# Performance work log

Hardware: AMD Instinct MI355X
Metric: run time of the kernel (lower is better)

The kernel has to match this reference:

```python
import jax, jax.numpy as jnp
import numpy as np

N_HEADS = 16


def setup_inputs() -> dict:
    key = jax.random.key(0)
    ks = jax.random.split(key, 9)
    B, S, D = 2, 2048, 1024
    s = 0.02
    return {
        "x": jax.random.normal(ks[0], (B, S, D), dtype=jnp.float32),
        "Wq": jax.random.normal(ks[1], (D, D), dtype=jnp.float32) * s,
        "bq": jax.random.normal(ks[2], (D,), dtype=jnp.float32) * s,
        "Wk": jax.random.normal(ks[3], (D, D), dtype=jnp.float32) * s,
        "bk": jax.random.normal(ks[4], (D,), dtype=jnp.float32) * s,
        "Wv": jax.random.normal(ks[5], (D, D), dtype=jnp.float32) * s,
        "bv": jax.random.normal(ks[6], (D,), dtype=jnp.float32) * s,
        "Wo": jax.random.normal(ks[7], (D, D), dtype=jnp.float32) * s,
        "bo": jax.random.normal(ks[8], (D,), dtype=jnp.float32) * s,
    }


def reference(x, Wq, bq, Wk, bk, Wv, bv, Wo, bo):
    B, S, D = x.shape
    H = N_HEADS
    hd = D // H
    # projections -> [B, H, S, hd]
    def heads(w, b):
        return (x @ w + b).reshape(B, S, H, hd).transpose(0, 2, 1, 3)
    Q, K, V = heads(Wq, bq), heads(Wk, bk), heads(Wv, bv)
    scores = jnp.einsum("bhqd,bhkd->bhqk", Q, K)
    causal = jnp.triu(jnp.ones((S, S), dtype=bool), k=1)  # True above diagonal
    scores = jnp.where(causal, -jnp.inf, scores)
    w = jax.nn.softmax(scores / jnp.sqrt(jnp.float32(hd)), axis=-1)
    ctx = jnp.einsum("bhqk,bhkd->bhqd", w, V).transpose(0, 2, 1, 3).reshape(B, S, D)
    return ctx @ Wo + bo
```

## Files before the change

### kernel.cpp

```cpp
#include <hip/hip_runtime.h>
#include <hip/hip_bf16.h>

typedef __attribute__((ext_vector_type(8))) short short8;
typedef __attribute__((ext_vector_type(4))) float floatx4;
typedef __attribute__((ext_vector_type(4))) int intx4;

#define D_MODEL 1024
#define SEQ     2048
#define NB      2
#define NH      16
#define HD      64
#define MROWS   4096
#define CZ      (0.125f * 1.44269504f)

__device__ __forceinline__ floatx4 mfma_bf16(short8 a, short8 b, floatx4 c) {
  return __builtin_amdgcn_mfma_f32_16x16x32_bf16(a, b, c, 0, 0, 0);
}

__device__ __forceinline__ void dma16(const __hip_bfloat16* g, __hip_bfloat16* l) {
  __builtin_amdgcn_global_load_lds(
      (const __attribute__((address_space(1))) void*)g,
      (__attribute__((address_space(3))) void*)l, 16, 0, 0);
}
#define WAIT_VM(n)  __asm__ __volatile__("s_waitcnt vmcnt(" #n ")" ::: "memory")
#define BARRIER()   __asm__ __volatile__("s_barrier" ::: "memory")
#define WAIT_LGKM() __asm__ __volatile__("s_waitcnt lgkmcnt(0)" ::: "memory")

__device__ __forceinline__ int pack2bf(float a, float b) {
  unsigned ua = __builtin_bit_cast(unsigned, a) + 0x8000u;
  unsigned ub = __builtin_bit_cast(unsigned, b) + 0x8000u;
  return (int)__builtin_amdgcn_perm(ub, ua, 0x07060302u);
}

__global__ void prep_kernel(const float* __restrict__ x, __hip_bfloat16* __restrict__ xb,
                            const float* __restrict__ W0, const float* __restrict__ W1,
                            const float* __restrict__ W2, const float* __restrict__ W3,
                            __hip_bfloat16* __restrict__ T0, __hip_bfloat16* __restrict__ T1,
                            __hip_bfloat16* __restrict__ T2, __hip_bfloat16* __restrict__ T3) {
  const int z = blockIdx.z;
  if (z == 4) {
    const int tid = threadIdx.y * 32 + threadIdx.x;
    const int base = ((blockIdx.y * 32 + blockIdx.x) * 256 + tid) * 16;
#pragma unroll
    for (int c = 0; c < 4; c++) {
      float4 v = *(const float4*)(x + base + c * 4);
      __hip_bfloat16 tmp[4];
      tmp[0] = __float2bfloat16(v.x);
      tmp[1] = __float2bfloat16(v.y);
      tmp[2] = __float2bfloat16(v.z);
      tmp[3] = __float2bfloat16(v.w);
      *(ushort4*)(xb + base + c * 4) = *(ushort4*)tmp;
    }
    return;
  }
  const float* W = (z == 0) ? W0 : (z == 1) ? W1 : (z == 2) ? W2 : W3;
  __hip_bfloat16* Wt = (z == 0) ? T0 : (z == 1) ? T1 : (z == 2) ? T2 : T3;
  __shared__ float tile[32][33];
  int k0 = blockIdx.x * 32, n0 = blockIdx.y * 32;
  int tx = threadIdx.x, ty = threadIdx.y;
#pragma unroll
  for (int i = 0; i < 4; i++)
    tile[ty + 8 * i][tx] = W[(size_t)(k0 + ty + 8 * i) * D_MODEL + n0 + tx];
  __syncthreads();
#pragma unroll
  for (int i = 0; i < 4; i++)
    Wt[(size_t)(n0 + ty + 8 * i) * D_MODEL + k0 + tx] = __float2bfloat16(tile[tx][ty + 8 * i]);
}

template <int MODE>
__global__ __launch_bounds__(256) void gemm_kernel(
    const __hip_bfloat16* __restrict__ X,
    const __hip_bfloat16* __restrict__ Wt0, const __hip_bfloat16* __restrict__ Wt1,
    const __hip_bfloat16* __restrict__ Wt2,
    const float* __restrict__ b0, const float* __restrict__ b1, const float* __restrict__ b2,
    void* __restrict__ out0, void* __restrict__ out1, void* __restrict__ out2) {
  constexpr int MT = (MODE == 0) ? 128 : 64;
  constexpr int I = MT / 32;
  constexpr int NKT = D_MODEL / 32;
  constexpr int SMEM_BYTES = 3 * (MT * 32 + 128 * 32) * 2;

  const int z = blockIdx.y;
  const __hip_bfloat16* Wt = (z == 0) ? Wt0 : (z == 1) ? Wt1 : Wt2;
  const float* bias = (z == 0) ? b0 : (z == 1) ? b1 : b2;
  void* outp = (z == 0) ? out0 : (z == 1) ? out1 : out2;
  const float scale = (MODE == 0 && z == 0) ? CZ : 1.f;

  __shared__ __attribute__((aligned(16))) char smem[SMEM_BYTES];
  __hip_bfloat16* As = (__hip_bfloat16*)smem;
  __hip_bfloat16* Bs = (__hip_bfloat16*)smem + 3 * MT * 32;
  float* Es = (float*)smem;

  const int n0 = blockIdx.x * 128;
  const int m0 = blockIdx.z * MT;
  const int t = threadIdx.x;
  const int lane = t & 63, w = t >> 6;
  const int wm = (w >> 1) * (MT / 2), wn = (w & 1) * 64;
  const int lr = lane & 15;
  const int lq = lane >> 4;

  const __hip_bfloat16* Xp = X + (size_t)m0 * D_MODEL;
  const __hip_bfloat16* Wp = Wt + (size_t)n0 * D_MODEL;

  const int lrow = lane >> 2;
  const int skg = (lane & 3) << 3;
  const int srowA = ((MT == 128) ? (w << 5) : (w << 4)) + lrow;
  const int sbA0 = (((MT == 128) ? (w << 5) : (w << 4)) << 5);
  const int sbA1 = sbA0 + (16 << 5);
  const int srowB = (w << 5) + lrow;
  const int sbB0 = ((w << 5) << 5);
  const int sbB1 = sbB0 + (16 << 5);

#define STAGE_G(kt_, buf_)                                                              \
  {                                                                                     \
    const int kn_ = (kt_) * 32;                                                         \
    __hip_bfloat16* A_ = As + (buf_) * (MT * 32);                                       \
    __hip_bfloat16* B_ = Bs + (buf_) * (128 * 32);                                      \
    dma16(Xp + (size_t)srowA * D_MODEL + kn_ + skg, A_ + sbA0);                         \
    if (MT == 128) dma16(Xp + (size_t)(srowA + 16) * D_MODEL + kn_ + skg, A_ + sbA1);   \
    dma16(Wp + (size_t)srowB * D_MODEL + kn_ + skg, B_ + sbB0);                         \
    dma16(Wp + (size_t)(srowB + 16) * D_MODEL + kn_ + skg, B_ + sbB1);                  \
  }

  floatx4 acc[I][4];
#pragma unroll
  for (int i = 0; i < I; i++)
#pragma unroll
    for (int j = 0; j < 4; j++) acc[i][j] = (floatx4){0.f, 0.f, 0.f, 0.f};

  STAGE_G(0, 0);
  STAGE_G(1, 1);

  int cb = 0;
  for (int kt = 0; kt < NKT; kt++) {
    if (kt < NKT - 1) {
      if constexpr (MODE == 0) WAIT_VM(4);
      else                     WAIT_VM(3);
    } else {
      WAIT_VM(0);
    }
    BARRIER();
    if (kt + 2 < NKT) {
      const int nb = (cb == 0) ? 2 : cb - 1;
      STAGE_G(kt + 2, nb);
    }
    const __hip_bfloat16* Ac = As + cb * (MT * 32);
    const __hip_bfloat16* Bc = Bs + cb * (128 * 32);
    short8 af[I], bfr[4];
#pragma unroll
    for (int i = 0; i < I; i++) af[i] = *(const short8*)&Ac[(wm + i * 16 + lr) * 32 + lq * 8];
#pragma unroll
    for (int j = 0; j < 4; j++) bfr[j] = *(const short8*)&Bc[(wn + j * 16 + lr) * 32 + lq * 8];
#pragma unroll
    for (int i = 0; i < I; i++)
#pragma unroll
      for (int j = 0; j < 4; j++) acc[i][j] = mfma_bf16(af[i], bfr[j], acc[i][j]);
    cb = (cb == 2) ? 0 : cb + 1;
  }
#undef STAGE_G

  float bvj[4];
#pragma unroll
  for (int j = 0; j < 4; j++) bvj[j] = bias[n0 + wn + j * 16 + lr];

  if constexpr (MODE == 1) {
    BARRIER();
#pragma unroll
    for (int i = 0; i < I; i++) {
      const int rowb = wm + i * 16 + lq * 4;
#pragma unroll
      for (int j = 0; j < 4; j++)
#pragma unroll
        for (int r = 0; r < 4; r++)
          Es[(rowb + r) * 132 + wn + j * 16 + lr] = acc[i][j][r] + bvj[j];
    }
    WAIT_LGKM();
    BARRIER();
    const int L = t >> 2, nseg = (t & 3) * 32;
    float* op = (float*)outp + (size_t)(m0 + L) * D_MODEL + n0 + nseg;
    const float* src = &Es[L * 132 + nseg];
#pragma unroll
    for (int k = 0; k < 8; k++) *(float4*)(op + 4 * k) = *(const float4*)(src + 4 * k);
  } else if (z != 2) {
    for (int c = 0; c < 2; c++) {
      BARRIER();
#pragma unroll
      for (int i2 = 0; i2 < 2; i2++) {
        const int i = 2 * c + i2;
        const int rowb = (w >> 1) * 32 + i2 * 16 + lq * 4;
#pragma unroll
        for (int j = 0; j < 4; j++)
#pragma unroll
          for (int r = 0; r < 4; r++)
            Es[(rowb + r) * 132 + wn + j * 16 + lr] = (acc[i][j][r] + bvj[j]) * scale;
      }
      WAIT_LGKM();
      BARRIER();
      const int L = t >> 2, nseg = (t & 3) * 32;
      const int m = m0 + ((L >> 5) << 6) + (c << 5) + (L & 31);
      const int bb = m >> 11, s = m & 2047;
      const int nn = n0 + nseg;
      __hip_bfloat16* op = (__hip_bfloat16*)outp +
          (((size_t)(bb * NH + (nn >> 6)) * SEQ + s) * HD + (nn & 63));
      const float* src = &Es[L * 132 + nseg];
#pragma unroll
      for (int k = 0; k < 4; k++) {
        intx4 pk;
        pk[0] = pack2bf(src[8 * k + 0], src[8 * k + 1]);
        pk[1] = pack2bf(src[8 * k + 2], src[8 * k + 3]);
        pk[2] = pack2bf(src[8 * k + 4], src[8 * k + 5]);
        pk[3] = pack2bf(src[8 * k + 6], src[8 * k + 7]);
        *(intx4*)(op + 8 * k) = pk;
      }
    }
  } else {
    for (int c = 0; c < 2; c++) {
      BARRIER();
#pragma unroll
      for (int j2 = 0; j2 < 2; j2++) {
        const int j = 2 * c + j2;
        const int nl = ((w & 1) << 5) + (j2 << 4) + lr;
#pragma unroll
        for (int i = 0; i < I; i++) {
          const int moff = (w >> 1) * 64 + i * 16 + lq * 4;
          floatx4 v = acc[i][j];
          v[0] += bvj[j]; v[1] += bvj[j]; v[2] += bvj[j]; v[3] += bvj[j];
          *(floatx4*)&Es[nl * 132 + moff] = v;
        }
      }
      WAIT_LGKM();
      BARRIER();
      const int nl = t >> 2, mseg = (t & 3) * 32;
      const int n = n0 + ((nl >> 5) << 6) + (c << 5) + (nl & 31);
      const int s0 = m0 & 2047, bb = m0 >> 11;
      __hip_bfloat16* op = (__hip_bfloat16*)outp +
          (((size_t)(bb * NH + (n >> 6)) * HD + (n & 63)) * SEQ + s0 + mseg);
      const float* src = &Es[nl * 132 + mseg];
#pragma unroll
      for (int k = 0; k < 4; k++) {
        intx4 pk;
        pk[0] = pack2bf(src[8 * k + 0], src[8 * k + 1]);
        pk[1] = pack2bf(src[8 * k + 2], src[8 * k + 3]);
        pk[2] = pack2bf(src[8 * k + 4], src[8 * k + 5]);
        pk[3] = pack2bf(src[8 * k + 6], src[8 * k + 7]);
        *(intx4*)(op + 8 * k) = pk;
      }
    }
  }
}

__global__ __launch_bounds__(256, 4) void attn_kernel(
    const __hip_bfloat16* __restrict__ Q, const __hip_bfloat16* __restrict__ Kg,
    const __hip_bfloat16* __restrict__ Vt, __hip_bfloat16* __restrict__ ctx) {
  const int bh = blockIdx.x;
  const int b = bh >> 4, h = bh & 15;
  const int qt = 31 - blockIdx.y;
  const int t = threadIdx.x, lane = t & 63, w = t >> 6;
  const int lr = lane & 15, lq = lane >> 4;
  const int wr = w & 1, wb = w >> 1;

  __shared__ __attribute__((aligned(16))) __hip_bfloat16 Ks[2][64 * 64];
  __shared__ __attribute__((aligned(16))) __hip_bfloat16 VTs[2][64 * 64];

  const __hip_bfloat16* Qb = Q + (size_t)bh * SEQ * HD;
  const __hip_bfloat16* Kb = Kg + (size_t)bh * SEQ * HD;
  const __hip_bfloat16* Vb = Vt + (size_t)bh * HD * SEQ;

  const int qrow0 = qt * 64 + wr * 32;

  short8 qf[2][2];
#pragma unroll
  for (int rt = 0; rt < 2; rt++)
#pragma unroll
    for (int ks = 0; ks < 2; ks++)
      qf[rt][ks] = *(const short8*)(Qb + (size_t)(qrow0 + rt * 16 + lr) * HD + ks * 32 + lq * 8);

  const int srow = (w << 4) + (lane >> 3);
  const int sgl = lane & 7;
  const int sb0 = (w << 4) << 6;
  const int sb1 = ((w << 4) + 8) << 6;

#define STAGE(tb, nb)                                                                  \
  {                                                                                    \
    const int r0 = srow, r1 = srow + 8;                                                \
    dma16(Kb + ((size_t)((tb) + r0) << 6) + ((sgl ^ (r0 & 7)) << 3), &Ks[nb][sb0]);    \
    dma16(Kb + ((size_t)((tb) + r1) << 6) + ((sgl ^ (r1 & 7)) << 3), &Ks[nb][sb1]);    \
    dma16(Vb + (size_t)r0 * SEQ + (tb) + ((sgl ^ (r0 & 7)) << 3), &VTs[nb][sb0]);      \
    dma16(Vb + (size_t)r1 * SEQ + (tb) + ((sgl ^ (r1 & 7)) << 3), &VTs[nb][sb1]);      \
  }

  const int nkt = qt + 1;
  STAGE(0, 0);

  floatx4 o[2][4];
#pragma unroll
  for (int rt = 0; rt < 2; rt++)
#pragma unroll
    for (int dt = 0; dt < 4; dt++) o[rt][dt] = (floatx4){0.f, 0.f, 0.f, 0.f};
  float ls[2] = {0.f, 0.f};

  const int idx0 = (lr + ((lq & 1) << 5)) << 2;
  const int idx1 = idx0 + 64;
  const bool hi = (lq >= 2);

  const int kfb0 = ((wb << 4) + lr) << 6;
  const int kg0 = ((lq ^ (lr & 7)) << 3);
  const int kg1 = (((4 + lq) ^ (lr & 7)) << 3);
  const int vg = ((((lq & 2) << 1) + (wb << 1) + (lq & 1)) ^ (lr & 7)) << 3;

  for (int kt = 0; kt < nkt; kt++) {
    WAIT_VM(0);
    BARRIER();
    if (kt + 1 < nkt) STAGE((kt + 1) << 6, (kt + 1) & 1);

    const int kw0 = (kt << 6) + (wb << 4);
    if (kw0 <= qrow0 + 31) {
      const __hip_bfloat16* Kc = Ks[kt & 1];
      const __hip_bfloat16* Vc = VTs[kt & 1];

      short8 kf[2][2];
#pragma unroll
      for (int nt = 0; nt < 2; nt++) {
        kf[0][nt] = *(const short8*)&Kc[(nt << 11) + kfb0 + kg0];
        kf[1][nt] = *(const short8*)&Kc[(nt << 11) + kfb0 + kg1];
      }
      floatx4 s[2][2];
#pragma unroll
      for (int rt = 0; rt < 2; rt++)
#pragma unroll
        for (int nt = 0; nt < 2; nt++) s[rt][nt] = (floatx4){0.f, 0.f, 0.f, 0.f};
#pragma unroll
      for (int ks = 0; ks < 2; ks++)
#pragma unroll
        for (int nt = 0; nt < 2; nt++) {
          s[0][nt] = mfma_bf16(kf[ks][nt], qf[0][ks], s[0][nt]);
          s[1][nt] = mfma_bf16(kf[ks][nt], qf[1][ks], s[1][nt]);
        }

      const bool need_mask = (kw0 + 47 > qrow0);
      int pkA[2][2], pkB[2][2];
#pragma unroll
      for (int rt = 0; rt < 2; rt++) {
        const int q = qrow0 + rt * 16 + lr;
#pragma unroll
        for (int nt = 0; nt < 2; nt++) {
          const int kbase = (kt << 6) + (nt << 5) + (wb << 4) + (lq << 2);
          float x0 = s[rt][nt][0], x1 = s[rt][nt][1], x2 = s[rt][nt][2], x3 = s[rt][nt][3];
          if (need_mask) {
            x0 = (kbase + 0 <= q) ? x0 : -1e30f;
            x1 = (kbase + 1 <= q) ? x1 : -1e30f;
            x2 = (kbase + 2 <= q) ? x2 : -1e30f;
            x3 = (kbase + 3 <= q) ? x3 : -1e30f;
          }
          const float p0 = __builtin_amdgcn_exp2f(x0);
          const float p1 = __builtin_amdgcn_exp2f(x1);
          const float p2 = __builtin_amdgcn_exp2f(x2);
          const float p3 = __builtin_amdgcn_exp2f(x3);
          ls[rt] += (p0 + p1) + (p2 + p3);
          pkA[rt][nt] = pack2bf(p0, p1);
          pkB[rt][nt] = pack2bf(p2, p3);
        }
      }

      short8 pf[2];
#pragma unroll
      for (int rt = 0; rt < 2; rt++) {
        int c0a = __builtin_amdgcn_ds_bpermute(idx0, pkA[rt][0]);
        int c0b = __builtin_amdgcn_ds_bpermute(idx0, pkA[rt][1]);
        int c1a = __builtin_amdgcn_ds_bpermute(idx0, pkB[rt][0]);
        int c1b = __builtin_amdgcn_ds_bpermute(idx0, pkB[rt][1]);
        int c2a = __builtin_amdgcn_ds_bpermute(idx1, pkA[rt][0]);
        int c2b = __builtin_amdgcn_ds_bpermute(idx1, pkA[rt][1]);
        int c3a = __builtin_amdgcn_ds_bpermute(idx1, pkB[rt][0]);
        int c3b = __builtin_amdgcn_ds_bpermute(idx1, pkB[rt][1]);
        intx4 bi;
        bi[0] = hi ? c0b : c0a;
        bi[1] = hi ? c1b : c1a;
        bi[2] = hi ? c2b : c2a;
        bi[3] = hi ? c3b : c3a;
        pf[rt] = __builtin_bit_cast(short8, bi);
      }
#pragma unroll
      for (int dt = 0; dt < 4; dt++) {
        short8 vf = *(const short8*)&Vc[(((dt << 4) + lr) << 6) + vg];
        o[0][dt] = mfma_bf16(vf, pf[0], o[0][dt]);
        o[1][dt] = mfma_bf16(vf, pf[1], o[1][dt]);
      }
    }
  }

  BARRIER();
  if (wb == 1) {
    float* d0 = (float*)&Ks[0][0];
    float* d1 = (float*)&Ks[1][0];
    float* dl = (float*)&VTs[0][0];
    const int base = (wr << 10) + (lane << 4);
#pragma unroll
    for (int dt = 0; dt < 4; dt++) *(floatx4*)&d0[base + (dt << 2)] = o[0][dt];
#pragma unroll
    for (int dt = 0; dt < 4; dt++) *(floatx4*)&d1[base + (dt << 2)] = o[1][dt];
    dl[(wr << 7) + (lane << 1)] = ls[0];
    dl[(wr << 7) + (lane << 1) + 1] = ls[1];
    WAIT_LGKM();
  }
  BARRIER();
  if (wb == 0) {
    const float* d0 = (const float*)&Ks[0][0];
    const float* d1 = (const float*)&Ks[1][0];
    const float* dl = (const float*)&VTs[0][0];
    const int base = (wr << 10) + (lane << 4);
#pragma unroll
    for (int dt = 0; dt < 4; dt++) {
      o[0][dt] += *(const floatx4*)&d0[base + (dt << 2)];
      o[1][dt] += *(const floatx4*)&d1[base + (dt << 2)];
    }
    ls[0] += dl[(wr << 7) + (lane << 1)];
    ls[1] += dl[(wr << 7) + (lane << 1) + 1];
    float inv[2];
#pragma unroll
    for (int rt = 0; rt < 2; rt++) {
      float v = ls[rt];
      v += __shfl_xor(v, 16);
      v += __shfl_xor(v, 32);
      inv[rt] = 1.f / v;
    }
#pragma unroll
    for (int rt = 0; rt < 2; rt++) {
      const int row = qrow0 + rt * 16 + lr;
      __hip_bfloat16* cp = ctx + (size_t)b * SEQ * D_MODEL + (size_t)row * D_MODEL + h * HD;
#pragma unroll
      for (int dt = 0; dt < 4; dt++) {
        ushort4 pk;
        __hip_bfloat16* pp = (__hip_bfloat16*)&pk;
#pragma unroll
        for (int r = 0; r < 4; r++) pp[r] = __float2bfloat16(o[rt][dt][r] * inv[rt]);
        *(ushort4*)(cp + (dt << 4) + (lq << 2)) = pk;
      }
    }
  }
#undef STAGE
}

extern "C" void kernel_launch(void* const* d_in, const int* in_sizes, int n_in,
                              void* d_out, int out_size, void* d_ws, size_t ws_size,
                              hipStream_t stream) {
  const float* x  = (const float*)d_in[0];
  const float* Wq = (const float*)d_in[1];
  const float* bq = (const float*)d_in[2];
  const float* Wk = (const float*)d_in[3];
  const float* bk = (const float*)d_in[4];
  const float* Wv = (const float*)d_in[5];
  const float* bv = (const float*)d_in[6];
  const float* Wo = (const float*)d_in[7];
  const float* bo = (const float*)d_in[8];

  char* ws = (char*)d_ws;
  const size_t MB = 1u << 20;
  __hip_bfloat16* xb  = (__hip_bfloat16*)(ws + 0 * MB);
  __hip_bfloat16* wtq = (__hip_bfloat16*)(ws + 8 * MB);
  __hip_bfloat16* wtk = (__hip_bfloat16*)(ws + 10 * MB);
  __hip_bfloat16* wtv = (__hip_bfloat16*)(ws + 12 * MB);
  __hip_bfloat16* wto = (__hip_bfloat16*)(ws + 14 * MB);
  __hip_bfloat16* qb  = (__hip_bfloat16*)(ws + 16 * MB);
  __hip_bfloat16* kb  = (__hip_bfloat16*)(ws + 24 * MB);
  __hip_bfloat16* vt  = (__hip_bfloat16*)(ws + 32 * MB);
  __hip_bfloat16* ctx = xb;

  prep_kernel<<<dim3(32, 32, 5), dim3(32, 8), 0, stream>>>(x, xb, Wq, Wk, Wv, Wo,
                                                           wtq, wtk, wtv, wto);
  gemm_kernel<0><<<dim3(8, 3, 32), 256, 0, stream>>>(xb, wtq, wtk, wtv, bq, bk, bv,
                                                     (void*)qb, (void*)kb, (void*)vt);
  attn_kernel<<<dim3(32, 32), 256, 0, stream>>>(qb, kb, vt, ctx);
  gemm_kernel<1><<<dim3(8, 1, 64), 256, 0, stream>>>(ctx, wto, wto, wto, bo, bo, bo,
                                                     d_out, d_out, d_out);
}
```

Baseline: 191.3 us.

## Remove P-fragment bpermute shuffles by remapping V reads; sum rows via MFMA

Reorders how V^T is read from LDS (two 8-byte reads per fragment with a new swizzle offset) so the exp'd scores can be used directly as the MFMA B-operand without the eight ds_bpermute cross-lane shuffles per row tile. Row sums of P are computed with an extra MFMA against a ones vector instead of scalar adds plus cross-lane shuffles at the end. P is packed using the hardware v_cvt_pk_bf16_f32 instruction instead of manual rounding with perm. This trades LDS permute traffic and VALU work for two extra MFMAs and narrower LDS reads per tile, and the row sum is now taken from the bf16-rounded P values.

```diff
diff --git a/kernel.cpp b/kernel.cpp
--- a/kernel.cpp
+++ b/kernel.cpp
@@ -4,6 +4,7 @@
 typedef __attribute__((ext_vector_type(8))) short short8;
 typedef __attribute__((ext_vector_type(4))) float floatx4;
 typedef __attribute__((ext_vector_type(4))) int intx4;
+typedef __attribute__((ext_vector_type(2))) int intx2;
 
 #define D_MODEL 1024
 #define SEQ     2048
@@ -30,6 +31,12 @@
   unsigned ua = __builtin_bit_cast(unsigned, a) + 0x8000u;
   unsigned ub = __builtin_bit_cast(unsigned, b) + 0x8000u;
   return (int)__builtin_amdgcn_perm(ub, ua, 0x07060302u);
+}
+
+__device__ __forceinline__ int cvtpk(float a, float b) {
+  int r;
+  __asm__("v_cvt_pk_bf16_f32 %0, %1, %2" : "=v"(r) : "v"(a), "v"(b));
+  return r;
 }
 
 __global__ void prep_kernel(const float* __restrict__ x, __hip_bfloat16* __restrict__ xb,
@@ -296,16 +303,19 @@
   for (int rt = 0; rt < 2; rt++)
 #pragma unroll
     for (int dt = 0; dt < 4; dt++) o[rt][dt] = (floatx4){0.f, 0.f, 0.f, 0.f};
-  float ls[2] = {0.f, 0.f};
-
-  const int idx0 = (lr + ((lq & 1) << 5)) << 2;
-  const int idx1 = idx0 + 64;
-  const bool hi = (lq >= 2);
+  floatx4 lsacc[2];
+  lsacc[0] = (floatx4){0.f, 0.f, 0.f, 0.f};
+  lsacc[1] = (floatx4){0.f, 0.f, 0.f, 0.f};
+
+  short8 ones;
+#pragma unroll
+  for (int j = 0; j < 8; j++) ones[j] = (short)0x3F80;
 
   const int kfb0 = ((wb << 4) + lr) << 6;
   const int kg0 = ((lq ^ (lr & 7)) << 3);
   const int kg1 = (((4 + lq) ^ (lr & 7)) << 3);
-  const int vg = ((((lq & 2) << 1) + (wb << 1) + (lq & 1)) ^ (lr & 7)) << 3;
+  const int vga = (((wb * 2 + (lq >> 1)) ^ (lr & 7)) << 3) + ((lq & 1) << 2);
+  const int vgb = (((4 + wb * 2 + (lq >> 1)) ^ (lr & 7)) << 3) + ((lq & 1) << 2);
 
   for (int kt = 0; kt < nkt; kt++) {
     WAIT_VM(0);
@@ -337,10 +347,11 @@
         }
 
       const bool need_mask = (kw0 + 47 > qrow0);
-      int pkA[2][2], pkB[2][2];
+      short8 pf[2];
 #pragma unroll
       for (int rt = 0; rt < 2; rt++) {
         const int q = qrow0 + rt * 16 + lr;
+        intx4 pk;
 #pragma unroll
         for (int nt = 0; nt < 2; nt++) {
           const int kbase = (kt << 6) + (nt << 5) + (wb << 4) + (lq << 2);
@@ -355,33 +366,22 @@
           const float p1 = __builtin_amdgcn_exp2f(x1);
           const float p2 = __builtin_amdgcn_exp2f(x2);
           const float p3 = __builtin_amdgcn_exp2f(x3);
-          ls[rt] += (p0 + p1) + (p2 + p3);
-          pkA[rt][nt] = pack2bf(p0, p1);
-          pkB[rt][nt] = pack2bf(p2, p3);
+          pk[2 * nt + 0] = cvtpk(p0, p1);
+          pk[2 * nt + 1] = cvtpk(p2, p3);
         }
-      }
-
-      short8 pf[2];
-#pragma unroll
-      for (int rt = 0; rt < 2; rt++) {
-        int c0a = __builtin_amdgcn_ds_bpermute(idx0, pkA[rt][0]);
-        int c0b = __builtin_amdgcn_ds_bpermute(idx0, pkA[rt][1]);
-        int c1a = __builtin_amdgcn_ds_bpermute(idx0, pkB[rt][0]);
-        int c1b = __builtin_amdgcn_ds_bpermute(idx0, pkB[rt][1]);
-        int c2a = __builtin_amdgcn_ds_bpermute(idx1, pkA[rt][0]);
-        int c2b = __builtin_amdgcn_ds_bpermute(idx1, pkA[rt][1]);
-        int c3a = __builtin_amdgcn_ds_bpermute(idx1, pkB[rt][0]);
-        int c3b = __builtin_amdgcn_ds_bpermute(idx1, pkB[rt][1]);
-        intx4 bi;
-        bi[0] = hi ? c0b : c0a;
-        bi[1] = hi ? c1b : c1a;
-        bi[2] = hi ? c2b : c2a;
-        bi[3] = hi ? c3b : c3a;
-        pf[rt] = __builtin_bit_cast(short8, bi);
-      }
+        pf[rt] = __builtin_bit_cast(short8, pk);
+      }
+
+      lsacc[0] = mfma_bf16(ones, pf[0], lsacc[0]);
+      lsacc[1] = mfma_bf16(ones, pf[1], lsacc[1]);
+
 #pragma unroll
       for (int dt = 0; dt < 4; dt++) {
-        short8 vf = *(const short8*)&Vc[(((dt << 4) + lr) << 6) + vg];
+        const int rb = ((dt << 4) + lr) << 6;
+        intx4 vi;
+        *(intx2*)&vi = *(const intx2*)&Vc[rb + vga];
+        *(((intx2*)&vi) + 1) = *(const intx2*)&Vc[rb + vgb];
+        short8 vf = __builtin_bit_cast(short8, vi);
         o[0][dt] = mfma_bf16(vf, pf[0], o[0][dt]);
         o[1][dt] = mfma_bf16(vf, pf[1], o[1][dt]);
       }
@@ -398,8 +398,8 @@
     for (int dt = 0; dt < 4; dt++) *(floatx4*)&d0[base + (dt << 2)] = o[0][dt];
 #pragma unroll
     for (int dt = 0; dt < 4; dt++) *(floatx4*)&d1[base + (dt << 2)] = o[1][dt];
-    dl[(wr << 7) + (lane << 1)] = ls[0];
-    dl[(wr << 7) + (lane << 1) + 1] = ls[1];
+    dl[(wr << 7) + (lane << 1)] = lsacc[0][0];
+    dl[(wr << 7) + (lane << 1) + 1] = lsacc[1][0];
     WAIT_LGKM();
   }
   BARRIER();
@@ -413,16 +413,9 @@
       o[0][dt] += *(const floatx4*)&d0[base + (dt << 2)];
       o[1][dt] += *(const floatx4*)&d1[base + (dt << 2)];
     }
-    ls[0] += dl[(wr << 7) + (lane << 1)];
-    ls[1] += dl[(wr << 7) + (lane << 1) + 1];
     float inv[2];
-#pragma unroll
-    for (int rt = 0; rt < 2; rt++) {
-      float v = ls[rt];
-      v += __shfl_xor(v, 16);
-      v += __shfl_xor(v, 32);
-      inv[rt] = 1.f / v;
-    }
+    inv[0] = 1.f / (lsacc[0][0] + dl[(wr << 7) + (lane << 1)]);
+    inv[1] = 1.f / (lsacc[1][0] + dl[(wr << 7) + (lane << 1) + 1]);
 #pragma unroll
     for (int rt = 0; rt < 2; rt++) {
       const int row = qrow0 + rt * 16 + lr;
```

After: 186.7 us. 2.4% less time.
